# Optimization experiments

Hardware: AMD Instinct MI355X
Metric: run time of the kernel (lower is better)

Reference implementation:

```python
import jax, jax.numpy as jnp
import numpy as np

D_BINS = 88
DEPTH_MIN, DEPTH_MAX = 1.0, 45.0
BN_EPS = 1e-5


def setup_inputs() -> dict:
    key = jax.random.key(0)
    ks = jax.random.split(key, 8)
    N, C, H, W = 12, 256, 32, 88
    CC = 128  # context channels
    return {
        "x": jax.random.normal(ks[0], (N, C, H, W), dtype=jnp.float32),
        "dnet_w": jax.random.normal(ks[1], (D_BINS + CC, C), dtype=jnp.float32) * 0.05,
        "dnet_b": jax.random.normal(ks[2], (D_BINS + CC,), dtype=jnp.float32) * 0.05,
        "proj_w": jax.random.normal(ks[3], (C, CC), dtype=jnp.float32) * 0.05,
        "bn_gamma": jax.random.uniform(ks[4], (C,), dtype=jnp.float32) + 0.5,
        "bn_beta": jax.random.normal(ks[5], (C,), dtype=jnp.float32) * 0.1,
        "bn_mean": jax.random.normal(ks[6], (C,), dtype=jnp.float32) * 0.1,
        "bn_var": jax.random.uniform(ks[7], (C,), dtype=jnp.float32) + 0.5,
    }


def reference(x, dnet_w, dnet_b, proj_w, bn_gamma, bn_beta, bn_mean, bn_var):
    # depth_net: 1x1 conv == per-pixel matmul over channels
    dc = jnp.einsum('nchw,oc->nohw', x, dnet_w) + dnet_b[None, :, None, None]
    depth_logits = dc[:, :D_BINS]          # [N, D, H, W]
    tran_feat = dc[:, D_BINS:]             # [N, CC, H, W]
    # context_proj (1x1 conv, no bias) + BatchNorm2d (inference) + exact GELU
    tran_feat = jnp.einsum('nkhw,ck->nchw', tran_feat, proj_w)
    inv_std = jax.lax.rsqrt(bn_var + BN_EPS)
    tran_feat = (tran_feat - bn_mean[None, :, None, None]) * (bn_gamma * inv_std)[None, :, None, None] \
                + bn_beta[None, :, None, None]
    tran_feat = jax.nn.gelu(tran_feat, approximate=False)
    depth_prob = jax.nn.softmax(depth_logits, axis=1)  # [N, D, H, W]
    depth_values = jnp.linspace(DEPTH_MIN, DEPTH_MAX, D_BINS)
    depth_weight = depth_values / depth_values.mean()  # [D]
    # collapse_z=True: bev[n,c,h,w] = tran_feat[n,c,h,w] * sum_d depth_prob[n,d,h,w]*w[d]
    # (fused form of the [N,C,D,H,W] outer-product volume followed by sum over D)
    s = jnp.einsum('ndhw,d->nhw', depth_prob, depth_weight)  # [N, H, W]
    bev = tran_feat * s[:, None, :, :]
    return bev, depth_logits, depth_prob
```

## Files before the change

### kernel.cpp

```cpp
#include <hip/hip_runtime.h>
#include <hip/hip_bf16.h>
#include <math.h>

#define C_IN 256
#define CC 128
#define NDEPTH 88
#define HW 2816
#define NB 12
#define TILE 32
#define NTILES 88
#define LOG_OFF   ((size_t)8650752)
#define PROB_OFF  ((size_t)11624448)

typedef __attribute__((ext_vector_type(8))) short bf16x8;
typedef __attribute__((ext_vector_type(4))) float f32x4;

__device__ __forceinline__ unsigned short f2bf(float f) {
    unsigned int u = __float_as_uint(f);
    unsigned int r = (u + 0x7fffu + ((u >> 16) & 1u)) >> 16;
    return (unsigned short)r;
}
__device__ __forceinline__ unsigned int pack2(float a, float b) {
    return (unsigned int)f2bf(a) | ((unsigned int)f2bf(b) << 16);
}

__global__ void prep_kernel(const float* __restrict__ dnet_w,
                            const float* __restrict__ proj_w,
                            const float* __restrict__ gamma,
                            const float* __restrict__ beta,
                            const float* __restrict__ mean,
                            const float* __restrict__ var,
                            unsigned short* __restrict__ w1d,
                            unsigned short* __restrict__ w1t,
                            unsigned short* __restrict__ projb,
                            float* __restrict__ scale,
                            float* __restrict__ shift) {
    const int tid = blockIdx.x * blockDim.x + threadIdx.x;
    const int total = 96 * 256 + 128 * 256 + 256 * 128;
    for (int idx = tid; idx < total; idx += gridDim.x * blockDim.x) {
        if (idx < 96 * 256) {
            int o = idx >> 8, c = idx & 255;
            w1d[idx] = (o < NDEPTH) ? f2bf(dnet_w[o * 256 + c]) : (unsigned short)0;
        } else if (idx < 96 * 256 + 128 * 256) {
            int j = idx - 96 * 256;
            w1t[j] = f2bf(dnet_w[(NDEPTH + (j >> 8)) * 256 + (j & 255)]);
        } else {
            int j = idx - 96 * 256 - 128 * 256;
            projb[j] = f2bf(proj_w[j]);
        }
    }
    if (tid < 256) {
        float sc = gamma[tid] * rsqrtf(var[tid] + 1e-5f);
        scale[tid] = sc;
        shift[tid] = beta[tid] - mean[tid] * sc;
    }
}

__global__ __launch_bounds__(256, 4)
void fused_kernel(const float* __restrict__ x,
                  const float* __restrict__ dnet_b,
                  const unsigned short* __restrict__ w1d,
                  const unsigned short* __restrict__ w1t,
                  const unsigned short* __restrict__ projb,
                  const float* __restrict__ scale,
                  const float* __restrict__ shift,
                  float* __restrict__ out) {
    __shared__ __align__(16) unsigned short xs[32 * 256];
    __shared__ __align__(16) unsigned short trs[2][16 * 128];
    __shared__ float ss[2][16];
    __shared__ float biasd[96];
    __shared__ float biast[128];
    __shared__ float sc_s[256];
    __shared__ float sh_s[256];

    const int bid = blockIdx.x;
    const int n   = bid / NTILES;
    const int hw0 = (bid % NTILES) * TILE;
    const int t    = threadIdx.x;
    const int lane = t & 63;
    const int wv   = t >> 6;
    const int strip = wv >> 1;
    const int role  = wv & 1;

    if (t < 96)       biasd[t] = (t < NDEPTH) ? dnet_b[t] : 0.f;
    else if (t < 224) biast[t - 96] = dnet_b[t - 8];
    sc_s[t] = scale[t];
    sh_s[t] = shift[t];

    {
        const int hwl = t & 31;
        const int cg  = t >> 5;
        const float* xb = x + (size_t)n * C_IN * HW + hw0 + hwl;
        #pragma unroll
        for (int cb = 0; cb < 4; ++cb) {
            const int c0 = cb * 64 + cg * 8;
            float f[8];
            #pragma unroll
            for (int j = 0; j < 8; ++j) f[j] = xb[(size_t)(c0 + j) * HW];
            uint4 v;
            v.x = pack2(f[0], f[1]);
            v.y = pack2(f[2], f[3]);
            v.z = pack2(f[4], f[5]);
            v.w = pack2(f[6], f[7]);
            const int csw = (c0 >> 3) ^ (hwl & 7);
            *reinterpret_cast<uint4*>(&xs[hwl * 256 + csw * 8]) = v;
        }
    }
    __syncthreads();

    const int g = lane >> 4;
    const int m = lane & 15;
    const int brow  = strip * 16 + m;
    const int hwcol = hw0 + strip * 16 + m;

    if (role == 0) {
        f32x4 accd[6];
        #pragma unroll
        for (int i = 0; i < 6; ++i) accd[i] = (f32x4){0.f, 0.f, 0.f, 0.f};
        #pragma unroll
        for (int ks = 0; ks < 8; ++ks) {
            const int k0 = ks * 32;
            const int csw = ((k0 >> 3) + g) ^ (brow & 7);
            bf16x8 b = *reinterpret_cast<const bf16x8*>(&xs[brow * 256 + csw * 8]);
            #pragma unroll
            for (int dt = 0; dt < 6; ++dt) {
                bf16x8 a = *reinterpret_cast<const bf16x8*>(&w1d[(dt * 16 + m) * 256 + k0 + g * 8]);
                accd[dt] = __builtin_amdgcn_mfma_f32_16x16x32_bf16(a, b, accd[dt], 0, 0, 0);
            }
        }

        float dv[6][4], ev[6][4];
        float mx = -1e30f;
        #pragma unroll
        for (int dt = 0; dt < 6; ++dt) {
            #pragma unroll
            for (int r = 0; r < 4; ++r) {
                const int o = dt * 16 + g * 4 + r;
                float v = accd[dt][r] + biasd[o];
                dv[dt][r] = v;
                if (o < NDEPTH) mx = fmaxf(mx, v);
            }
        }
        mx = fmaxf(mx, __shfl_xor(mx, 16));
        mx = fmaxf(mx, __shfl_xor(mx, 32));
        float sum = 0.f;
        #pragma unroll
        for (int dt = 0; dt < 6; ++dt) {
            #pragma unroll
            for (int r = 0; r < 4; ++r) {
                const int o = dt * 16 + g * 4 + r;
                float e = (o < NDEPTH) ? __expf(dv[dt][r] - mx) : 0.f;
                ev[dt][r] = e;
                sum += e;
            }
        }
        sum += __shfl_xor(sum, 16);
        sum += __shfl_xor(sum, 32);
        const float inv = 1.0f / sum;

        float sp = 0.f;
        #pragma unroll
        for (int dt = 0; dt < 6; ++dt) {
            #pragma unroll
            for (int r = 0; r < 4; ++r) {
                const int o = dt * 16 + g * 4 + r;
                if (o < NDEPTH)
                    sp += ev[dt][r] * inv * ((1.f + (float)o * (44.f / 87.f)) * (1.f / 23.f));
            }
        }
        sp += __shfl_xor(sp, 16);
        sp += __shfl_xor(sp, 32);
        if (lane < 16) ss[strip][m] = sp;

        float* lg = out + LOG_OFF  + (size_t)n * NDEPTH * HW + hwcol;
        float* pb = out + PROB_OFF + (size_t)n * NDEPTH * HW + hwcol;
        #pragma unroll
        for (int dt = 0; dt < 6; ++dt) {
            #pragma unroll
            for (int r = 0; r < 4; ++r) {
                const int o = dt * 16 + g * 4 + r;
                if (o < NDEPTH) {
                    lg[(size_t)o * HW] = dv[dt][r];
                    pb[(size_t)o * HW] = ev[dt][r] * inv;
                }
            }
        }
    } else {
        f32x4 acct[8];
        #pragma unroll
        for (int i = 0; i < 8; ++i) acct[i] = (f32x4){0.f, 0.f, 0.f, 0.f};
        #pragma unroll
        for (int ks = 0; ks < 8; ++ks) {
            const int k0 = ks * 32;
            const int csw = ((k0 >> 3) + g) ^ (brow & 7);
            bf16x8 b = *reinterpret_cast<const bf16x8*>(&xs[brow * 256 + csw * 8]);
            #pragma unroll
            for (int tt = 0; tt < 8; ++tt) {
                bf16x8 a = *reinterpret_cast<const bf16x8*>(&w1t[(tt * 16 + m) * 256 + k0 + g * 8]);
                acct[tt] = __builtin_amdgcn_mfma_f32_16x16x32_bf16(a, b, acct[tt], 0, 0, 0);
            }
        }
        unsigned short* tw = &trs[strip][0];
        #pragma unroll
        for (int tt = 0; tt < 8; ++tt) {
            const int cb = tt * 16 + g * 4;
            float v0 = acct[tt][0] + biast[cb + 0];
            float v1 = acct[tt][1] + biast[cb + 1];
            float v2 = acct[tt][2] + biast[cb + 2];
            float v3 = acct[tt][3] + biast[cb + 3];
            const int csw = (cb >> 3) ^ (m & 7);
            uint2 pkd;
            pkd.x = pack2(v0, v1);
            pkd.y = pack2(v2, v3);
            *reinterpret_cast<uint2*>(&tw[m * 128 + csw * 8 + (g & 1) * 4]) = pkd;
        }
    }
    __syncthreads();

    f32x4 acc2[8];
    #pragma unroll
    for (int i = 0; i < 8; ++i) acc2[i] = (f32x4){0.f, 0.f, 0.f, 0.f};
    {
        const unsigned short* tw = &trs[strip][0];
        const int ctb = role * 8;
        #pragma unroll
        for (int ks = 0; ks < 4; ++ks) {
            const int k0 = ks * 32;
            const int csw = ((k0 >> 3) + g) ^ (m & 7);
            bf16x8 b = *reinterpret_cast<const bf16x8*>(&tw[m * 128 + csw * 8]);
            #pragma unroll
            for (int ct = 0; ct < 8; ++ct) {
                bf16x8 a = *reinterpret_cast<const bf16x8*>(&projb[((ctb + ct) * 16 + m) * 128 + k0 + g * 8]);
                acc2[ct] = __builtin_amdgcn_mfma_f32_16x16x32_bf16(a, b, acc2[ct], 0, 0, 0);
            }
        }
    }

    {
        const float sp = ss[strip][m];
        float* bev = out + (size_t)n * C_IN * HW + hwcol;
        const int ctb = role * 8;
        #pragma unroll
        for (int ct = 0; ct < 8; ++ct) {
            #pragma unroll
            for (int r = 0; r < 4; ++r) {
                const int cc = (ctb + ct) * 16 + g * 4 + r;
                float v  = acc2[ct][r] * sc_s[cc] + sh_s[cc];
                float ge = 0.5f * v * (1.f + erff(v * 0.70710678118f));
                bev[(size_t)cc * HW] = ge * sp;
            }
        }
    }
}

extern "C" void kernel_launch(void* const* d_in, const int* in_sizes, int n_in,
                              void* d_out, int out_size, void* d_ws, size_t ws_size,
                              hipStream_t stream) {
    const float* x      = (const float*)d_in[0];
    const float* dnet_w = (const float*)d_in[1];
    const float* dnet_b = (const float*)d_in[2];
    const float* proj_w = (const float*)d_in[3];
    const float* gamma  = (const float*)d_in[4];
    const float* beta   = (const float*)d_in[5];
    const float* mean   = (const float*)d_in[6];
    const float* var    = (const float*)d_in[7];
    float* out = (float*)d_out;

    char* ws = (char*)d_ws;
    unsigned short* w1d   = (unsigned short*)ws;
    unsigned short* w1t   = (unsigned short*)(ws + 49152);
    unsigned short* projb = (unsigned short*)(ws + 49152 + 65536);
    float* scale = (float*)(ws + 49152 + 65536 + 65536);
    float* shift = scale + 256;

    prep_kernel<<<96, 256, 0, stream>>>(dnet_w, proj_w, gamma, beta, mean, var,
                                        w1d, w1t, projb, scale, shift);
    fused_kernel<<<NB * NTILES, 256, 0, stream>>>(x, dnet_b, w1d, w1t, projb,
                                                  scale, shift, out);
}
```

Baseline: 161.0 us.

## Split K across two wave groups with 512-thread blocks and use tanh-form GELU

```diff
diff --git a/kernel.cpp b/kernel.cpp
--- a/kernel.cpp
+++ b/kernel.cpp
@@ -22,6 +22,13 @@
 }
 __device__ __forceinline__ unsigned int pack2(float a, float b) {
     return (unsigned int)f2bf(a) | ((unsigned int)f2bf(b) << 16);
+}
+__device__ __forceinline__ void bar_lgkm() {
+    asm volatile("s_waitcnt lgkmcnt(0)\n\ts_barrier" ::: "memory");
+}
+__device__ __forceinline__ float gelu_fast(float v) {
+    float u = v * (1.5957691216f + 0.07135481283f * v * v);
+    return v / (1.f + __expf(-u));
 }
 
 __global__ void prep_kernel(const float* __restrict__ dnet_w,
@@ -56,7 +63,7 @@
     }
 }
 
-__global__ __launch_bounds__(256, 4)
+__global__ __launch_bounds__(512, 6)
 void fused_kernel(const float* __restrict__ x,
                   const float* __restrict__ dnet_b,
                   const unsigned short* __restrict__ w1d,
@@ -65,7 +72,7 @@
                   const float* __restrict__ scale,
                   const float* __restrict__ shift,
                   float* __restrict__ out) {
-    __shared__ __align__(16) unsigned short xs[32 * 256];
+    __shared__ __align__(16) char buf[28672];
     __shared__ __align__(16) unsigned short trs[2][16 * 128];
     __shared__ float ss[2][16];
     __shared__ float biasd[96];
@@ -73,27 +80,31 @@
     __shared__ float sc_s[256];
     __shared__ float sh_s[256];
 
+    unsigned short* xs = (unsigned short*)buf;
+    f32x4* part = (f32x4*)buf;
+
     const int bid = blockIdx.x;
     const int n   = bid / NTILES;
     const int hw0 = (bid % NTILES) * TILE;
     const int t    = threadIdx.x;
     const int lane = t & 63;
     const int wv   = t >> 6;
-    const int strip = wv >> 1;
-    const int role  = wv & 1;
+    const int khalf = wv >> 2;
+    const int sub   = wv & 3;
+    const int strip = sub >> 1;
+    const int role  = sub & 1;
 
     if (t < 96)       biasd[t] = (t < NDEPTH) ? dnet_b[t] : 0.f;
     else if (t < 224) biast[t - 96] = dnet_b[t - 8];
-    sc_s[t] = scale[t];
-    sh_s[t] = shift[t];
+    if (t < 256) { sc_s[t] = scale[t]; sh_s[t] = shift[t]; }
 
     {
         const int hwl = t & 31;
         const int cg  = t >> 5;
         const float* xb = x + (size_t)n * C_IN * HW + hw0 + hwl;
         #pragma unroll
-        for (int cb = 0; cb < 4; ++cb) {
-            const int c0 = cb * 64 + cg * 8;
+        for (int cb = 0; cb < 2; ++cb) {
+            const int c0 = cb * 128 + cg * 8;
             float f[8];
             #pragma unroll
             for (int j = 0; j < 8; ++j) f[j] = xb[(size_t)(c0 + j) * HW];
@@ -106,7 +117,7 @@
             *reinterpret_cast<uint4*>(&xs[hwl * 256 + csw * 8]) = v;
         }
     }
-    __syncthreads();
+    bar_lgkm();
 
     const int g = lane >> 4;
     const int m = lane & 15;
@@ -118,8 +129,8 @@
         #pragma unroll
         for (int i = 0; i < 6; ++i) accd[i] = (f32x4){0.f, 0.f, 0.f, 0.f};
         #pragma unroll
-        for (int ks = 0; ks < 8; ++ks) {
-            const int k0 = ks * 32;
+        for (int ksl = 0; ksl < 4; ++ksl) {
+            const int k0 = (khalf * 4 + ksl) * 32;
             const int csw = ((k0 >> 3) + g) ^ (brow & 7);
             bf16x8 b = *reinterpret_cast<const bf16x8*>(&xs[brow * 256 + csw * 8]);
             #pragma unroll
@@ -128,60 +139,64 @@
                 accd[dt] = __builtin_amdgcn_mfma_f32_16x16x32_bf16(a, b, accd[dt], 0, 0, 0);
             }
         }
-
-        float dv[6][4], ev[6][4];
-        float mx = -1e30f;
-        #pragma unroll
-        for (int dt = 0; dt < 6; ++dt) {
-            #pragma unroll
-            for (int r = 0; r < 4; ++r) {
-                const int o = dt * 16 + g * 4 + r;
-                float v = accd[dt][r] + biasd[o];
-                dv[dt][r] = v;
-                if (o < NDEPTH) mx = fmaxf(mx, v);
-            }
-        }
-        mx = fmaxf(mx, __shfl_xor(mx, 16));
-        mx = fmaxf(mx, __shfl_xor(mx, 32));
-        float sum = 0.f;
-        #pragma unroll
-        for (int dt = 0; dt < 6; ++dt) {
-            #pragma unroll
-            for (int r = 0; r < 4; ++r) {
-                const int o = dt * 16 + g * 4 + r;
-                float e = (o < NDEPTH) ? __expf(dv[dt][r] - mx) : 0.f;
-                ev[dt][r] = e;
-                sum += e;
-            }
-        }
-        sum += __shfl_xor(sum, 16);
-        sum += __shfl_xor(sum, 32);
-        const float inv = 1.0f / sum;
-
-        float sp = 0.f;
-        #pragma unroll
-        for (int dt = 0; dt < 6; ++dt) {
-            #pragma unroll
-            for (int r = 0; r < 4; ++r) {
-                const int o = dt * 16 + g * 4 + r;
-                if (o < NDEPTH)
-                    sp += ev[dt][r] * inv * ((1.f + (float)o * (44.f / 87.f)) * (1.f / 23.f));
-            }
-        }
-        sp += __shfl_xor(sp, 16);
-        sp += __shfl_xor(sp, 32);
-        if (lane < 16) ss[strip][m] = sp;
-
-        float* lg = out + LOG_OFF  + (size_t)n * NDEPTH * HW + hwcol;
-        float* pb = out + PROB_OFF + (size_t)n * NDEPTH * HW + hwcol;
-        #pragma unroll
-        for (int dt = 0; dt < 6; ++dt) {
-            #pragma unroll
-            for (int r = 0; r < 4; ++r) {
-                const int o = dt * 16 + g * 4 + r;
-                if (o < NDEPTH) {
-                    lg[(size_t)o * HW] = dv[dt][r];
-                    pb[(size_t)o * HW] = ev[dt][r] * inv;
+        bar_lgkm();
+        if (khalf == 1) {
+            #pragma unroll
+            for (int dt = 0; dt < 6; ++dt)
+                part[(strip * 14 + dt) * 64 + lane] = accd[dt];
+        }
+        bar_lgkm();
+        if (khalf == 0) {
+            #pragma unroll
+            for (int dt = 0; dt < 6; ++dt)
+                accd[dt] += part[(strip * 14 + dt) * 64 + lane];
+            #pragma unroll
+            for (int dt = 0; dt < 6; ++dt) {
+                #pragma unroll
+                for (int r = 0; r < 4; ++r)
+                    accd[dt][r] += biasd[dt * 16 + g * 4 + r];
+            }
+            float mx = -1e30f;
+            #pragma unroll
+            for (int dt = 0; dt < 6; ++dt) {
+                #pragma unroll
+                for (int r = 0; r < 4; ++r) {
+                    const int o = dt * 16 + g * 4 + r;
+                    if (o < NDEPTH) mx = fmaxf(mx, accd[dt][r]);
+                }
+            }
+            mx = fmaxf(mx, __shfl_xor(mx, 16));
+            mx = fmaxf(mx, __shfl_xor(mx, 32));
+            float sum = 0.f, spn = 0.f;
+            #pragma unroll
+            for (int dt = 0; dt < 6; ++dt) {
+                #pragma unroll
+                for (int r = 0; r < 4; ++r) {
+                    const int o = dt * 16 + g * 4 + r;
+                    if (o < NDEPTH) {
+                        float e = __expf(accd[dt][r] - mx);
+                        sum += e;
+                        spn += e * ((1.f + (float)o * (44.f / 87.f)) * (1.f / 23.f));
+                    }
+                }
+            }
+            sum += __shfl_xor(sum, 16);
+            sum += __shfl_xor(sum, 32);
+            spn += __shfl_xor(spn, 16);
+            spn += __shfl_xor(spn, 32);
+            const float inv = 1.0f / sum;
+            if (lane < 16) ss[strip][m] = spn * inv;
+            float* lg = out + LOG_OFF  + (size_t)n * NDEPTH * HW + hwcol;
+            float* pb = out + PROB_OFF + (size_t)n * NDEPTH * HW + hwcol;
+            #pragma unroll
+            for (int dt = 0; dt < 6; ++dt) {
+                #pragma unroll
+                for (int r = 0; r < 4; ++r) {
+                    const int o = dt * 16 + g * 4 + r;
+                    if (o < NDEPTH) {
+                        lg[(size_t)o * HW] = accd[dt][r];
+                        pb[(size_t)o * HW] = __expf(accd[dt][r] - mx) * inv;
+                    }
                 }
             }
         }
@@ -190,8 +205,8 @@
         #pragma unroll
         for (int i = 0; i < 8; ++i) acct[i] = (f32x4){0.f, 0.f, 0.f, 0.f};
         #pragma unroll
-        for (int ks = 0; ks < 8; ++ks) {
-            const int k0 = ks * 32;
+        for (int ksl = 0; ksl < 4; ++ksl) {
+            const int k0 = (khalf * 4 + ksl) * 32;
             const int csw = ((k0 >> 3) + g) ^ (brow & 7);
             bf16x8 b = *reinterpret_cast<const bf16x8*>(&xs[brow * 256 + csw * 8]);
             #pragma unroll
@@ -200,36 +215,50 @@
                 acct[tt] = __builtin_amdgcn_mfma_f32_16x16x32_bf16(a, b, acct[tt], 0, 0, 0);
             }
         }
-        unsigned short* tw = &trs[strip][0];
-        #pragma unroll
-        for (int tt = 0; tt < 8; ++tt) {
-            const int cb = tt * 16 + g * 4;
-            float v0 = acct[tt][0] + biast[cb + 0];
-            float v1 = acct[tt][1] + biast[cb + 1];
-            float v2 = acct[tt][2] + biast[cb + 2];
-            float v3 = acct[tt][3] + biast[cb + 3];
-            const int csw = (cb >> 3) ^ (m & 7);
-            uint2 pkd;
-            pkd.x = pack2(v0, v1);
-            pkd.y = pack2(v2, v3);
-            *reinterpret_cast<uint2*>(&tw[m * 128 + csw * 8 + (g & 1) * 4]) = pkd;
-        }
-    }
-    __syncthreads();
-
-    f32x4 acc2[8];
+        bar_lgkm();
+        if (khalf == 1) {
+            #pragma unroll
+            for (int tt = 0; tt < 8; ++tt)
+                part[(strip * 14 + 6 + tt) * 64 + lane] = acct[tt];
+        }
+        bar_lgkm();
+        if (khalf == 0) {
+            #pragma unroll
+            for (int tt = 0; tt < 8; ++tt)
+                acct[tt] += part[(strip * 14 + 6 + tt) * 64 + lane];
+            unsigned short* tw = &trs[strip][0];
+            #pragma unroll
+            for (int tt = 0; tt < 8; ++tt) {
+                const int cb = tt * 16 + g * 4;
+                float v0 = acct[tt][0] + biast[cb + 0];
+                float v1 = acct[tt][1] + biast[cb + 1];
+                float v2 = acct[tt][2] + biast[cb + 2];
+                float v3 = acct[tt][3] + biast[cb + 3];
+                const int csw = (cb >> 3) ^ (m & 7);
+                uint2 pkd;
+                pkd.x = pack2(v0, v1);
+                pkd.y = pack2(v2, v3);
+                *reinterpret_cast<uint2*>(&tw[m * 128 + csw * 8 + (g & 1) * 4]) = pkd;
+            }
+        }
+    }
+    bar_lgkm();
+
+    const int strip2 = wv >> 2;
+    const int ctb    = (wv & 3) * 4;
+    const int hwcol2 = hw0 + strip2 * 16 + m;
+    f32x4 acc2[4];
     #pragma unroll
-    for (int i = 0; i < 8; ++i) acc2[i] = (f32x4){0.f, 0.f, 0.f, 0.f};
+    for (int i = 0; i < 4; ++i) acc2[i] = (f32x4){0.f, 0.f, 0.f, 0.f};
     {
-        const unsigned short* tw = &trs[strip][0];
-        const int ctb = role * 8;
+        const unsigned short* tw = &trs[strip2][0];
         #pragma unroll
         for (int ks = 0; ks < 4; ++ks) {
             const int k0 = ks * 32;
             const int csw = ((k0 >> 3) + g) ^ (m & 7);
             bf16x8 b = *reinterpret_cast<const bf16x8*>(&tw[m * 128 + csw * 8]);
             #pragma unroll
-            for (int ct = 0; ct < 8; ++ct) {
+            for (int ct = 0; ct < 4; ++ct) {
                 bf16x8 a = *reinterpret_cast<const bf16x8*>(&projb[((ctb + ct) * 16 + m) * 128 + k0 + g * 8]);
                 acc2[ct] = __builtin_amdgcn_mfma_f32_16x16x32_bf16(a, b, acc2[ct], 0, 0, 0);
             }
@@ -237,17 +266,15 @@
     }
 
     {
-        const float sp = ss[strip][m];
-        float* bev = out + (size_t)n * C_IN * HW + hwcol;
-        const int ctb = role * 8;
-        #pragma unroll
-        for (int ct = 0; ct < 8; ++ct) {
+        const float sp = ss[strip2][m];
+        float* bev = out + (size_t)n * C_IN * HW + hwcol2;
+        #pragma unroll
+        for (int ct = 0; ct < 4; ++ct) {
             #pragma unroll
             for (int r = 0; r < 4; ++r) {
                 const int cc = (ctb + ct) * 16 + g * 4 + r;
                 float v  = acc2[ct][r] * sc_s[cc] + sh_s[cc];
-                float ge = 0.5f * v * (1.f + erff(v * 0.70710678118f));
-                bev[(size_t)cc * HW] = ge * sp;
+                bev[(size_t)cc * HW] = gelu_fast(v) * sp;
             }
         }
     }
@@ -275,6 +302,6 @@
 
     prep_kernel<<<96, 256, 0, stream>>>(dnet_w, proj_w, gamma, beta, mean, var,
                                         w1d, w1t, projb, scale, shift);
-    fused_kernel<<<NB * NTILES, 256, 0, stream>>>(x, dnet_b, w1d, w1t, projb,
+    fused_kernel<<<NB * NTILES, 512, 0, stream>>>(x, dnet_b, w1d, w1t, projb,
                                                   scale, shift, out);
 }
```

Result: faster. 155.4 us (-3.5%).
